# Kernel optimization log

Measured on AMD Instinct MI355X. Metric: run time of the kernel, lower is better.

The kernel has to match this reference:

```python
import jax, jax.numpy as jnp
import numpy as np

B, H = 1_000_000, 18
TEMPERATURE = 1.0
EPS = 1e-8
NEG = -1e9  # stand-in for -inf that keeps logaddexp/exp finite


def setup_inputs() -> dict:
    key = jax.random.key(0)
    k1, k2, k3 = jax.random.split(key, 3)
    scores = jax.random.normal(k1, (B, H), dtype=jnp.float32)
    rankings = jax.random.randint(k2, (B, H), 0, 18, dtype=jnp.int32)
    mask = jax.random.randint(k3, (B, H), 0, 2, dtype=jnp.int32).astype(bool)
    return {"scores": scores, "rankings": rankings, "mask": mask}


def reference(scores, rankings, mask):
    # valid horses: masked-in and ranking >= 0
    valid = mask & (rankings >= 0)                      # (B, H) bool
    num_horses = scores.shape[1]

    # Stable sort valid horses to the front, ordered by ranking (Plackett-Luce order).
    sort_key = jnp.where(valid, rankings, num_horses + 1)
    order = jnp.argsort(sort_key, axis=1)               # stable
    s = jnp.take_along_axis(jnp.clip(scores, -10.0, 10.0), order, axis=1) / TEMPERATURE
    v = jnp.take_along_axis(valid, order, axis=1)
    s = jnp.where(v, s, NEG)                            # invalid horses contribute exp(-1e9)=0

    # Reverse cumulative logsumexp replaces the O(n^2) sequential softmax peel:
    # lse[i] = logsumexp(s[i:])  ->  log P(pick i-th) = s[i] - lse[i]
    lse = jax.lax.associative_scan(jnp.logaddexp, s, reverse=True, axis=1)
    prob = jnp.clip(jnp.exp(s - lse), EPS, 1.0 - EPS)   # matches original per-step prob clamp

    n = jnp.sum(valid, axis=1)                          # (B,) valid horse count
    # positions 0 .. n-2 contribute (last pick is deterministic)
    pos_ok = jnp.arange(num_horses)[None, :] < (n - 1)[:, None]
    race_loss = jnp.sum(jnp.where(pos_ok, -jnp.log(prob), 0.0), axis=1)

    race_valid = n >= 2                                 # races with <2 valid horses skipped
    num = jnp.sum(jnp.where(race_valid, race_loss, 0.0))
    den = jnp.sum(race_valid)
    return jnp.where(den > 0, num / jnp.maximum(den, 1).astype(num.dtype), jnp.float32(0.0))
```

## Files before the change

### kernel.cpp

```cpp
#include <hip/hip_runtime.h>
#include <stdint.h>

#define H 18
#define TPB 256
#define NBLK 2048
#define DETECT_WORDS 16384

__device__ __forceinline__ void ce(unsigned long long& x, unsigned long long& y) {
    unsigned long long a = x, b = y;
    bool lt = a < b;
    x = lt ? a : b;
    y = lt ? b : a;
}

__global__ __launch_bounds__(256) void detect_mask(const unsigned int* __restrict__ mw,
                                                   int* __restrict__ flag) {
    unsigned int acc = 0;
    for (int i = threadIdx.x; i < DETECT_WORDS; i += 256) {
        acc |= (mw[i] > 1u) ? 1u : 0u;
    }
    __shared__ int sh;
    if (threadIdx.x == 0) sh = 0;
    __syncthreads();
    if (__any(acc != 0) && (threadIdx.x & 63) == 0) atomicOr(&sh, 1);
    __syncthreads();
    if (threadIdx.x == 0) *flag = sh;
}

__global__ __launch_bounds__(TPB) void pl_main(const float* __restrict__ scores,
                                               const int* __restrict__ rankings,
                                               const unsigned char* __restrict__ mask8,
                                               const int* __restrict__ flag,
                                               int B,
                                               float* __restrict__ partial_loss,
                                               int* __restrict__ partial_cnt) {
    const bool u8mode = (*flag != 0);
    float th_loss = 0.0f;
    int th_cnt = 0;

    for (int race = blockIdx.x * TPB + threadIdx.x; race < B; race += gridDim.x * TPB) {
        const float2* s2 = reinterpret_cast<const float2*>(scores + (size_t)race * H);
        const int2*   r2 = reinterpret_cast<const int2*>(rankings + (size_t)race * H);

        int mv[H];
        if (u8mode) {
            const uchar2* m2 = reinterpret_cast<const uchar2*>(mask8 + (size_t)race * H);
#pragma unroll
            for (int q = 0; q < H / 2; ++q) {
                uchar2 t = m2[q];
                mv[2 * q]     = t.x;
                mv[2 * q + 1] = t.y;
            }
        } else {
            const int2* m2 = reinterpret_cast<const int2*>(
                reinterpret_cast<const int*>(mask8) + (size_t)race * H);
#pragma unroll
            for (int q = 0; q < H / 2; ++q) {
                int2 t = m2[q];
                mv[2 * q]     = t.x;
                mv[2 * q + 1] = t.y;
            }
        }

        float s[H];
        int key[H];
        float m = -1e30f;
        int n = 0;

#pragma unroll
        for (int q = 0; q < H / 2; ++q) {
            float2 sv = s2[q];
            int2   rv = r2[q];
            float s0 = fminf(fmaxf(sv.x, -10.0f), 10.0f);
            float s1 = fminf(fmaxf(sv.y, -10.0f), 10.0f);
            bool v0 = (mv[2 * q] != 0) && (rv.x >= 0);
            bool v1 = (mv[2 * q + 1] != 0) && (rv.y >= 0);
            s[2 * q]     = s0;
            s[2 * q + 1] = s1;
            key[2 * q]     = v0 ? (rv.x & 31) : 31;
            key[2 * q + 1] = v1 ? (rv.y & 31) : 31;
            if (v0) { n++; m = fmaxf(m, s0); }
            if (v1) { n++; m = fmaxf(m, s1); }
        }

        unsigned long long a[H];
#pragma unroll
        for (int j = 0; j < H; ++j) {
            unsigned int hi = ((unsigned int)key[j] << 5) | (unsigned int)j;
            a[j] = ((unsigned long long)hi << 32) | (unsigned long long)__float_as_uint(s[j]);
        }

#pragma unroll
        for (int p = 1; p < H; p <<= 1) {
#pragma unroll
            for (int k = p; k >= 1; k >>= 1) {
#pragma unroll
                for (int j = k % p; j + k < H; j += 2 * k) {
#pragma unroll
                    for (int i = 0; i < k; ++i) {
                        if (i + j + k < H) {
                            if ((i + j) / (2 * p) == (i + j + k) / (2 * p)) {
                                ce(a[i + j], a[i + j + k]);
                            }
                        }
                    }
                }
            }
        }

        if (n >= 2) {
            float run = 0.0f;
            float loss = 0.0f;
            int cnt = 0;
#pragma unroll
            for (int q = H - 1; q >= 0; --q) {
                unsigned long long w = a[q];
                unsigned int hi = (unsigned int)(w >> 32);
                int kq = (int)(hi >> 5);
                if (kq < 31) {
                    float sv = __uint_as_float((unsigned int)w);
                    float e = __expf(sv - m);
                    run += e;
                    cnt++;
                    if (cnt > 1) {
                        float t = m + __logf(run) - sv;
                        t = fminf(fmaxf(t, 1.0000000e-8f), 18.420680744f);
                        loss += t;
                    }
                }
            }
            th_loss += loss;
            th_cnt += 1;
        }
    }

#pragma unroll
    for (int off = 32; off >= 1; off >>= 1) {
        th_loss += __shfl_down(th_loss, off);
        th_cnt  += __shfl_down(th_cnt, off);
    }
    __shared__ float ls[TPB / 64];
    __shared__ int   cs[TPB / 64];
    int wid = threadIdx.x >> 6;
    int lane = threadIdx.x & 63;
    if (lane == 0) { ls[wid] = th_loss; cs[wid] = th_cnt; }
    __syncthreads();
    if (threadIdx.x == 0) {
        float L = 0.0f;
        int C = 0;
#pragma unroll
        for (int w = 0; w < TPB / 64; ++w) { L += ls[w]; C += cs[w]; }
        partial_loss[blockIdx.x] = L;
        partial_cnt[blockIdx.x]  = C;
    }
}

__global__ __launch_bounds__(1024) void pl_final(const float* __restrict__ partial_loss,
                                                 const int* __restrict__ partial_cnt,
                                                 int nb, float* __restrict__ out) {
    float L = 0.0f;
    int C = 0;
    for (int i = threadIdx.x; i < nb; i += 1024) {
        L += partial_loss[i];
        C += partial_cnt[i];
    }
#pragma unroll
    for (int off = 32; off >= 1; off >>= 1) {
        L += __shfl_down(L, off);
        C += __shfl_down(C, off);
    }
    __shared__ float ls[1024 / 64];
    __shared__ int   cs[1024 / 64];
    int wid = threadIdx.x >> 6;
    int lane = threadIdx.x & 63;
    if (lane == 0) { ls[wid] = L; cs[wid] = C; }
    __syncthreads();
    if (threadIdx.x == 0) {
        float tl = 0.0f;
        int tc = 0;
#pragma unroll
        for (int w = 0; w < 1024 / 64; ++w) { tl += ls[w]; tc += cs[w]; }
        out[0] = (tc > 0) ? (tl / (float)tc) : 0.0f;
    }
}

extern "C" void kernel_launch(void* const* d_in, const int* in_sizes, int n_in,
                              void* d_out, int out_size, void* d_ws, size_t ws_size,
                              hipStream_t stream) {
    const float*         scores   = (const float*)d_in[0];
    const int*           rankings = (const int*)d_in[1];
    const unsigned char* mask     = (const unsigned char*)d_in[2];

    int B = in_sizes[0] / H;
    int nb = (B + TPB - 1) / TPB;
    if (nb > NBLK) nb = NBLK;

    int*   flag = (int*)d_ws;
    float* pl   = (float*)((char*)d_ws + 256);
    int*   pc   = (int*)((char*)d_ws + 256 + (size_t)NBLK * sizeof(float));

    detect_mask<<<1, 256, 0, stream>>>((const unsigned int*)mask, flag);
    pl_main<<<nb, TPB, 0, stream>>>(scores, rankings, mask, flag, B, pl, pc);
    pl_final<<<1, 1024, 0, stream>>>(pl, pc, nb, (float*)d_out);
}
```

Measured before the change: 229.8 us.

## Stage race data through LDS with coalesced loads and fold mask detection into main kernel

```diff
diff --git a/kernel.cpp b/kernel.cpp
--- a/kernel.cpp
+++ b/kernel.cpp
@@ -3,8 +3,7 @@
 
 #define H 18
 #define TPB 256
-#define NBLK 2048
-#define DETECT_WORDS 16384
+#define RPB 256
 
 __device__ __forceinline__ void ce(unsigned long long& x, unsigned long long& y) {
     unsigned long long a = x, b = y;
@@ -13,81 +12,81 @@
     y = lt ? b : a;
 }
 
-__global__ __launch_bounds__(256) void detect_mask(const unsigned int* __restrict__ mw,
-                                                   int* __restrict__ flag) {
-    unsigned int acc = 0;
-    for (int i = threadIdx.x; i < DETECT_WORDS; i += 256) {
-        acc |= (mw[i] > 1u) ? 1u : 0u;
-    }
-    __shared__ int sh;
-    if (threadIdx.x == 0) sh = 0;
-    __syncthreads();
-    if (__any(acc != 0) && (threadIdx.x & 63) == 0) atomicOr(&sh, 1);
-    __syncthreads();
-    if (threadIdx.x == 0) *flag = sh;
-}
-
 __global__ __launch_bounds__(TPB) void pl_main(const float* __restrict__ scores,
                                                const int* __restrict__ rankings,
                                                const unsigned char* __restrict__ mask8,
-                                               const int* __restrict__ flag,
                                                int B,
                                                float* __restrict__ partial_loss,
                                                int* __restrict__ partial_cnt) {
-    const bool u8mode = (*flag != 0);
+    __shared__ float2 sS[RPB * 9];
+    __shared__ unsigned short sK[RPB * 9];
+    __shared__ int sFlag;
+    __shared__ float ls[TPB / 64];
+    __shared__ int   cs[TPB / 64];
+
+    const int t = threadIdx.x;
+    const int lane = t & 63;
+    const int wid = t >> 6;
+
+    if (t == 0) sFlag = 0;
+    __syncthreads();
+    {
+        unsigned int w = reinterpret_cast<const unsigned int*>(mask8)[t];
+        if (__any(w > 1u) && lane == 0) atomicOr(&sFlag, 1);
+    }
+    __syncthreads();
+    const bool u8mode = (sFlag != 0);
+
+    const int race0 = blockIdx.x * RPB;
+    const int limit = min(RPB, B - race0);
+    const int nflat2 = limit * 9;
+
+    const float2* s2 = reinterpret_cast<const float2*>(scores) + (size_t)race0 * 9;
+    const int2*   r2 = reinterpret_cast<const int2*>(rankings) + (size_t)race0 * 9;
+
+#pragma unroll
+    for (int k = 0; k < 9; ++k) {
+        int f2 = k * TPB + t;
+        if (f2 < nflat2) {
+            sS[f2] = s2[f2];
+            int2 rv = r2[f2];
+            int m0, m1;
+            if (u8mode) {
+                uchar2 mb = *reinterpret_cast<const uchar2*>(
+                    mask8 + (size_t)race0 * 18 + 2 * (size_t)f2);
+                m0 = mb.x; m1 = mb.y;
+            } else {
+                int2 mb = reinterpret_cast<const int2*>(mask8)[(size_t)race0 * 9 + f2];
+                m0 = mb.x; m1 = mb.y;
+            }
+            unsigned int k0 = (m0 != 0 && rv.x >= 0) ? (unsigned int)min(rv.x, 30) : 31u;
+            unsigned int k1 = (m1 != 0 && rv.y >= 0) ? (unsigned int)min(rv.y, 30) : 31u;
+            sK[f2] = (unsigned short)(k0 | (k1 << 8));
+        }
+    }
+    __syncthreads();
+
     float th_loss = 0.0f;
     int th_cnt = 0;
 
-    for (int race = blockIdx.x * TPB + threadIdx.x; race < B; race += gridDim.x * TPB) {
-        const float2* s2 = reinterpret_cast<const float2*>(scores + (size_t)race * H);
-        const int2*   r2 = reinterpret_cast<const int2*>(rankings + (size_t)race * H);
-
-        int mv[H];
-        if (u8mode) {
-            const uchar2* m2 = reinterpret_cast<const uchar2*>(mask8 + (size_t)race * H);
-#pragma unroll
-            for (int q = 0; q < H / 2; ++q) {
-                uchar2 t = m2[q];
-                mv[2 * q]     = t.x;
-                mv[2 * q + 1] = t.y;
-            }
-        } else {
-            const int2* m2 = reinterpret_cast<const int2*>(
-                reinterpret_cast<const int*>(mask8) + (size_t)race * H);
-#pragma unroll
-            for (int q = 0; q < H / 2; ++q) {
-                int2 t = m2[q];
-                mv[2 * q]     = t.x;
-                mv[2 * q + 1] = t.y;
-            }
-        }
-
-        float s[H];
-        int key[H];
+    if (t < limit) {
+        unsigned long long a[H];
         float m = -1e30f;
         int n = 0;
-
 #pragma unroll
-        for (int q = 0; q < H / 2; ++q) {
-            float2 sv = s2[q];
-            int2   rv = r2[q];
+        for (int j = 0; j < 9; ++j) {
+            float2 sv = sS[t * 9 + j];
+            unsigned int kp = sK[t * 9 + j];
             float s0 = fminf(fmaxf(sv.x, -10.0f), 10.0f);
             float s1 = fminf(fmaxf(sv.y, -10.0f), 10.0f);
-            bool v0 = (mv[2 * q] != 0) && (rv.x >= 0);
-            bool v1 = (mv[2 * q + 1] != 0) && (rv.y >= 0);
-            s[2 * q]     = s0;
-            s[2 * q + 1] = s1;
-            key[2 * q]     = v0 ? (rv.x & 31) : 31;
-            key[2 * q + 1] = v1 ? (rv.y & 31) : 31;
-            if (v0) { n++; m = fmaxf(m, s0); }
-            if (v1) { n++; m = fmaxf(m, s1); }
-        }
-
-        unsigned long long a[H];
-#pragma unroll
-        for (int j = 0; j < H; ++j) {
-            unsigned int hi = ((unsigned int)key[j] << 5) | (unsigned int)j;
-            a[j] = ((unsigned long long)hi << 32) | (unsigned long long)__float_as_uint(s[j]);
+            unsigned int k0 = kp & 0xffu;
+            unsigned int k1 = (kp >> 8) & 0xffu;
+            if (k0 < 31u) { n++; m = fmaxf(m, s0); }
+            if (k1 < 31u) { n++; m = fmaxf(m, s1); }
+            unsigned int hi0 = (k0 << 5) | (unsigned int)(2 * j);
+            unsigned int hi1 = (k1 << 5) | (unsigned int)(2 * j + 1);
+            a[2 * j]     = ((unsigned long long)hi0 << 32) | (unsigned long long)__float_as_uint(s0);
+            a[2 * j + 1] = ((unsigned long long)hi1 << 32) | (unsigned long long)__float_as_uint(s1);
         }
 
 #pragma unroll
@@ -123,14 +122,14 @@
                     run += e;
                     cnt++;
                     if (cnt > 1) {
-                        float t = m + __logf(run) - sv;
-                        t = fminf(fmaxf(t, 1.0000000e-8f), 18.420680744f);
-                        loss += t;
+                        float tt = m + __logf(run) - sv;
+                        tt = fminf(fmaxf(tt, 1.0000000e-8f), 18.420680744f);
+                        loss += tt;
                     }
                 }
             }
-            th_loss += loss;
-            th_cnt += 1;
+            th_loss = loss;
+            th_cnt = 1;
         }
     }
 
@@ -139,13 +138,9 @@
         th_loss += __shfl_down(th_loss, off);
         th_cnt  += __shfl_down(th_cnt, off);
     }
-    __shared__ float ls[TPB / 64];
-    __shared__ int   cs[TPB / 64];
-    int wid = threadIdx.x >> 6;
-    int lane = threadIdx.x & 63;
     if (lane == 0) { ls[wid] = th_loss; cs[wid] = th_cnt; }
     __syncthreads();
-    if (threadIdx.x == 0) {
+    if (t == 0) {
         float L = 0.0f;
         int C = 0;
 #pragma unroll
@@ -192,14 +187,11 @@
     const unsigned char* mask     = (const unsigned char*)d_in[2];
 
     int B = in_sizes[0] / H;
-    int nb = (B + TPB - 1) / TPB;
-    if (nb > NBLK) nb = NBLK;
+    int nb = (B + RPB - 1) / RPB;
 
-    int*   flag = (int*)d_ws;
-    float* pl   = (float*)((char*)d_ws + 256);
-    int*   pc   = (int*)((char*)d_ws + 256 + (size_t)NBLK * sizeof(float));
+    float* pl = (float*)d_ws;
+    int*   pc = (int*)((char*)d_ws + ((size_t)nb * sizeof(float) + 255 & ~(size_t)255));
 
-    detect_mask<<<1, 256, 0, stream>>>((const unsigned int*)mask, flag);
-    pl_main<<<nb, TPB, 0, stream>>>(scores, rankings, mask, flag, B, pl, pc);
+    pl_main<<<nb, TPB, 0, stream>>>(scores, rankings, mask, B, pl, pc);
     pl_final<<<1, 1024, 0, stream>>>(pl, pc, nb, (float*)d_out);
 }
```

After: 227.7 us. Within noise of the previous version (-0.9%).
